# Kernel tuning notes

Measured on AMD Instinct MI355X. Metric: run time of the kernel, lower is better.

The kernel has to match this reference:

```python
import jax, jax.numpy as jnp
import numpy as np

KH = KW = 3
SH = SW = 1
PH = PW = 1


def _im2col(x, kh, kw, sh, sw, ph, pw):
    # x: [N, C, H, W] -> cols: [N, C*kh*kw, H_out*W_out], ordering (C, kh, kw)
    N, C, H, W = x.shape
    H_out = (H + 2 * ph - kh) // sh + 1
    W_out = (W + 2 * pw - kw) // sw + 1
    x_pad = jnp.pad(x, ((0, 0), (0, 0), (ph, ph), (pw, pw)))
    # fixed small loop over kernel offsets (kh*kw = 9), strided slices
    patches = [x_pad[:, :, i:i + sh * H_out:sh, j:j + sw * W_out:sw]
               for i in range(kh) for j in range(kw)]  # each [N, C, H_out, W_out]
    cols = jnp.stack(patches, axis=2)  # [N, C, kh*kw, H_out, W_out]
    cols = cols.reshape(N, C * kh * kw, H_out * W_out)
    return cols, H_out, W_out


def setup_inputs() -> dict:
    key = jax.random.key(0)
    k1, k2, k3 = jax.random.split(key, 3)
    x = jax.random.normal(k1, (16, 128, 56, 56), dtype=jnp.float32)
    weight = jax.random.normal(k2, (256, 128, 3, 3), dtype=jnp.float32) * 0.05
    fan_in = 128 * 3 * 3
    bound = 1.0 / fan_in ** 0.5
    bias = jax.random.uniform(k3, (256,), dtype=jnp.float32, minval=-bound, maxval=bound)
    return {"x": x, "weight": weight, "bias": bias}


def reference(x, weight, bias):
    # im2col unfold + (analog) matmul conv; noise_cfg=None -> plain matmul
    cols, H_out, W_out = _im2col(x, KH, KW, SH, SW, PH, PW)  # [N, K, L]
    N = cols.shape[0]
    Cout = weight.shape[0]
    Wmat = weight.reshape(Cout, -1)  # [Cout, K], K = C*kh*kw
    # y[n, l, o] = sum_k cols[n, k, l] * Wmat[o, k]  (AnalogMatMulFn without noise)
    y = jnp.einsum('nkl,ok->nol', cols, Wmat)  # [N, Cout, L]
    y = y.reshape(N, Cout, H_out, W_out)
    y = y + bias[None, :, None, None]
    return y
```

## Files before the change

### kernel.cpp

```cpp
#include <hip/hip_runtime.h>
#include <hip/hip_bf16.h>
#include <stdint.h>


typedef __attribute__((ext_vector_type(8))) short short8;
typedef __attribute__((ext_vector_type(4))) float floatx4;

__device__ static inline void gload_lds16(const void* g, void* l) {
  typedef const __attribute__((address_space(1))) unsigned int* gp_t;
  typedef __attribute__((address_space(3))) unsigned int* lp_t;
  __builtin_amdgcn_global_load_lds((gp_t)(uintptr_t)g, (lp_t)(uint32_t)(uintptr_t)l,
                                   16, 0, 0);
}

__global__ __launch_bounds__(256)
void pre_kernel(const float* __restrict__ x, const float* __restrict__ wsrc,
                __hip_bfloat16* __restrict__ xp, __hip_bfloat16* __restrict__ wt) {
  const int b = blockIdx.x;
  if (b < 16 * 58) {
    const int n = b / 58, hp = b % 58;
    __hip_bfloat16* dst = xp + (size_t)(n * 58 + hp) * 58 * 128;
    if (hp == 0 || hp == 57) {
      const uint4 z = {0, 0, 0, 0};
      uint4* p = (uint4*)dst;
      for (int i = threadIdx.x; i < 928; i += 256) p[i] = z;
      return;
    }
    const int h = hp - 1;
    __shared__ float tile[128][57];
    const float* src = x + (size_t)n * (128 * 3136) + h * 56;
    for (int i = threadIdx.x; i < 128 * 14; i += 256) {
      const int c = i / 14, q = i - c * 14;
      const float4 v = ((const float4*)(src + (size_t)c * 3136))[q];
      tile[c][4 * q + 0] = v.x;
      tile[c][4 * q + 1] = v.y;
      tile[c][4 * q + 2] = v.z;
      tile[c][4 * q + 3] = v.w;
    }
    __syncthreads();
    if (threadIdx.x < 32) {
      const uint4 z = {0, 0, 0, 0};
      const int col = (threadIdx.x >> 4) * 57;
      ((uint4*)(dst + (size_t)col * 128))[threadIdx.x & 15] = z;
    }
    __hip_bfloat16* di = dst + 128;
    for (int i = threadIdx.x; i < 56 * 16; i += 256) {
      const int w = i >> 4, c8 = (i & 15) * 8;
      union { uint4 u; __hip_bfloat16 hh[8]; } pk;
#pragma unroll
      for (int j = 0; j < 8; ++j) pk.hh[j] = __float2bfloat16(tile[c8 + j][w]);
      *(uint4*)(di + (size_t)w * 128 + c8) = pk.u;
    }
  } else {
    const int base = (b - 928) * 256 + threadIdx.x;
    for (int t = base; t < 256 * 9 * 128; t += 36 * 256) {
      const int e = t & 7;
      const int rr = (t >> 3) & 15;
      const int q = (t >> 7) & 3;
      const int ks = (t >> 9) & 1;
      const int ch = (t >> 10) & 1;
      const int t11 = t >> 11;
      const int kq = t11 % 9;
      const int g = t11 / 9;
      const int cout = g * 16 + rr;
      const int c = ch * 64 + ks * 32 + q * 8 + e;
      wt[t] = __float2bfloat16(wsrc[(size_t)(cout * 128 + c) * 9 + kq]);
    }
  }
}

__global__ __launch_bounds__(256, 3)
void conv_gemm_kernel(const __hip_bfloat16* __restrict__ xp,
                      const __hip_bfloat16* __restrict__ wt,
                      const float* __restrict__ bias,
                      float* __restrict__ out) {
  __shared__ __align__(16) char smem[49152];

  const int tid = threadIdx.x;
  const int lane = tid & 63;
  const int wave = tid >> 6;
  const int col = lane & 15;
  const int quad = lane >> 4;

  const int id = blockIdx.x;
  const int xcd = id & 7;
  const int r = id >> 3;
  const int nt_ = xcd * 98 + r;
  const int n0 = nt_ * 64;

  const int nimg0 = n0 / 3136;
  const int rem0 = n0 - nimg0 * 3136;
  const int hh0 = rem0 / 56;
  const int ww0 = rem0 - hh0 * 56;
  const int P0 = (nimg0 * 58 + hh0) * 58 + ww0;
  const char* pbase = (const char*)xp + (size_t)P0 * 256;

#pragma unroll
  for (int i = 0; i < 12; ++i) {
    const int j = i * 256 + tid;
    const int row = j >> 4;
    const int slot = j & 15;
    gload_lds16(pbase + row * 256 + ((slot ^ (row & 7)) << 4),
                smem + i * 4096 + wave * 1024);
  }

  const char* wtb = (const char*)wt;
  const char* pA = wtb + (size_t)(wave * 4) * 36864 + lane * 16;

  int rbase[4];
#pragma unroll
  for (int nt = 0; nt < 4; ++nt) {
    const int pix = n0 + nt * 16 + col;
    const int ni = pix / 3136;
    const int re = pix - ni * 3136;
    const int ph = re / 56;
    const int pw = re - ph * 56;
    rbase[nt] = (ni * 58 + ph) * 58 + pw - P0;
  }

  floatx4 acc[4][4];
#pragma unroll
  for (int a = 0; a < 4; ++a)
#pragma unroll
    for (int c = 0; c < 4; ++c) acc[a][c] = (floatx4)0.f;

  __syncthreads();

#pragma unroll
  for (int s = 0; s < 18; ++s) {
    const int kq = s >> 1, ch = s & 1;
    const int kh = kq / 3;
    const int tofs = kh * 58 + (kq - kh * 3);
    const int aofs = kq * 4096 + ch * 2048;

    short8 af[4][2];
#pragma unroll
    for (int mt = 0; mt < 4; ++mt)
#pragma unroll
      for (int ks = 0; ks < 2; ++ks)
        af[mt][ks] = *(const short8*)(pA + mt * 36864 + aofs + ks * 1024);

    short8 bf[4][2];
#pragma unroll
    for (int nt = 0; nt < 4; ++nt) {
      const int rowB = rbase[nt] + tofs;
#pragma unroll
      for (int ks = 0; ks < 2; ++ks) {
        const int cB = ch * 8 + ks * 4 + quad;
        const int pos = cB ^ (rowB & 7);
        bf[nt][ks] = *(const short8*)(smem + rowB * 256 + (pos << 4));
      }
    }

#pragma unroll
    for (int ks = 0; ks < 2; ++ks)
#pragma unroll
      for (int mt = 0; mt < 4; ++mt)
#pragma unroll
        for (int nt = 0; nt < 4; ++nt)
          acc[mt][nt] = __builtin_amdgcn_mfma_f32_16x16x32_bf16(
              af[mt][ks], bf[nt][ks], acc[mt][nt], 0, 0, 0);
  }

  const int rb = quad * 4;
#pragma unroll
  for (int nt = 0; nt < 4; ++nt) {
    const int pix = n0 + nt * 16 + col;
    const int nimg = pix / 3136;
    const int rem = pix - nimg * 3136;
    float* op = out + (size_t)nimg * (256 * 3136) + rem;
#pragma unroll
    for (int mt = 0; mt < 4; ++mt) {
      const int mb = wave * 64 + mt * 16 + rb;
#pragma unroll
      for (int rr = 0; rr < 4; ++rr) {
        op[(size_t)(mb + rr) * 3136] = acc[mt][nt][rr] + bias[mb + rr];
      }
    }
  }
}

__global__ __launch_bounds__(256)
void direct_conv_kernel(const float* __restrict__ x, const float* __restrict__ wgt,
                        const float* __restrict__ bias, float* __restrict__ out) {
  const long t = (long)blockIdx.x * 256 + threadIdx.x;
  if (t >= 16L * 256 * 3136) return;
  const int w = t % 56;
  const int h = (t / 56) % 56;
  const int o = (t / 3136) % 256;
  const int n = t / (256L * 3136);
  float s = bias[o];
  for (int c = 0; c < 128; ++c)
    for (int kh = 0; kh < 3; ++kh) {
      const int hh = h + kh - 1;
      if (hh < 0 || hh >= 56) continue;
      for (int kw = 0; kw < 3; ++kw) {
        const int ww = w + kw - 1;
        if (ww < 0 || ww >= 56) continue;
        s += x[((size_t)(n * 128 + c) * 56 + hh) * 56 + ww] *
             wgt[((size_t)(o * 128 + c) * 3 + kh) * 3 + kw];
      }
    }
  out[t] = s;
}

extern "C" void kernel_launch(void* const* d_in, const int* in_sizes, int n_in,
                              void* d_out, int out_size, void* d_ws, size_t ws_size,
                              hipStream_t stream) {
  const float* x = (const float*)d_in[0];
  const float* w = (const float*)d_in[1];
  const float* b = (const float*)d_in[2];
  float* out = (float*)d_out;

  const size_t xp_bytes = (size_t)16 * 58 * 58 * 128 * 2;
  const size_t wt_bytes = (size_t)256 * 9 * 128 * 2;

  if (ws_size >= xp_bytes + wt_bytes) {
    __hip_bfloat16* xp = (__hip_bfloat16*)d_ws;
    __hip_bfloat16* wt = (__hip_bfloat16*)((char*)d_ws + xp_bytes);
    hipLaunchKernelGGL(pre_kernel, dim3(16 * 58 + 36), dim3(256), 0, stream,
                       x, w, xp, wt);
    hipLaunchKernelGGL(conv_gemm_kernel, dim3(784), dim3(256), 0, stream,
                       xp, wt, b, out);
  } else {
    const long total = 16L * 256 * 3136;
    hipLaunchKernelGGL(direct_conv_kernel, dim3((unsigned)((total + 255) / 256)),
                       dim3(256), 0, stream, x, w, b, out);
  }
}
```

Before: 128.8 us.

## Tile output pixels as 8x8 spatial blocks to shrink LDS halo

Each block now covers an 8x8 spatial tile instead of 64 consecutive pixels along rows. The 10x10 halo needs only 100 padded rows in LDS instead of 192, so LDS drops from 48KB to 25KB. Launch bounds are raised to allow 4 blocks per CU. Output stores become strided 8-wide segments rather than 64 contiguous floats, which may reduce write coalescing.

```diff
diff --git a/kernel.cpp b/kernel.cpp
--- a/kernel.cpp
+++ b/kernel.cpp
@@ -69,12 +69,12 @@
   }
 }
 
-__global__ __launch_bounds__(256, 3)
+__global__ __launch_bounds__(256, 4)
 void conv_gemm_kernel(const __hip_bfloat16* __restrict__ xp,
                       const __hip_bfloat16* __restrict__ wt,
                       const float* __restrict__ bias,
                       float* __restrict__ out) {
-  __shared__ __align__(16) char smem[49152];
+  __shared__ __align__(16) char smem[25600];
 
   const int tid = threadIdx.x;
   const int lane = tid & 63;
@@ -85,37 +85,41 @@
   const int id = blockIdx.x;
   const int xcd = id & 7;
   const int r = id >> 3;
-  const int nt_ = xcd * 98 + r;
-  const int n0 = nt_ * 64;
-
-  const int nimg0 = n0 / 3136;
-  const int rem0 = n0 - nimg0 * 3136;
-  const int hh0 = rem0 / 56;
-  const int ww0 = rem0 - hh0 * 56;
-  const int P0 = (nimg0 * 58 + hh0) * 58 + ww0;
-  const char* pbase = (const char*)xp + (size_t)P0 * 256;
-
-#pragma unroll
-  for (int i = 0; i < 12; ++i) {
-    const int j = i * 256 + tid;
-    const int row = j >> 4;
-    const int slot = j & 15;
-    gload_lds16(pbase + row * 256 + ((slot ^ (row & 7)) << 4),
-                smem + i * 4096 + wave * 1024);
+  const int t = xcd * 98 + r;
+  const int nimg = t / 49;
+  const int ti = t - nimg * 49;
+  const int th = ti / 7;
+  const int tw = ti - th * 7;
+  const int h0 = th * 8, w0 = tw * 8;
+
+  const char* pbase = (const char*)xp +
+                      ((size_t)(nimg * 58 + h0) * 58 + w0) * 256;
+
+#pragma unroll
+  for (int i = 0; i < 7; ++i) {
+    if (i < 6 || tid < 64) {
+      const int j = i * 256 + tid;
+      const int row = j >> 4;
+      const int hh = row / 10;
+      const int ww = row - hh * 10;
+      const int slot = j & 15;
+      const int srcb = (slot ^ (row & 7)) << 4;
+      gload_lds16(pbase + (hh * 58 + ww) * 256 + srcb,
+                  smem + i * 4096 + wave * 1024);
+    }
   }
 
   const char* wtb = (const char*)wt;
   const char* pA = wtb + (size_t)(wave * 4) * 36864 + lane * 16;
 
-  int rbase[4];
+  int rbase[4], pixofs[4];
 #pragma unroll
   for (int nt = 0; nt < 4; ++nt) {
-    const int pix = n0 + nt * 16 + col;
-    const int ni = pix / 3136;
-    const int re = pix - ni * 3136;
-    const int ph = re / 56;
-    const int pw = re - ph * 56;
-    rbase[nt] = (ni * 58 + ph) * 58 + pw - P0;
+    const int idx = nt * 16 + col;
+    const int lh = idx >> 3;
+    const int lw = idx & 7;
+    rbase[nt] = lh * 10 + lw;
+    pixofs[nt] = (h0 + lh) * 56 + (w0 + lw);
   }
 
   floatx4 acc[4][4];
@@ -130,7 +134,7 @@
   for (int s = 0; s < 18; ++s) {
     const int kq = s >> 1, ch = s & 1;
     const int kh = kq / 3;
-    const int tofs = kh * 58 + (kq - kh * 3);
+    const int tofs = kh * 10 + (kq - kh * 3);
     const int aofs = kq * 4096 + ch * 2048;
 
     short8 af[4][2];
@@ -162,16 +166,12 @@
               af[mt][ks], bf[nt][ks], acc[mt][nt], 0, 0, 0);
   }
 
-  const int rb = quad * 4;
 #pragma unroll
   for (int nt = 0; nt < 4; ++nt) {
-    const int pix = n0 + nt * 16 + col;
-    const int nimg = pix / 3136;
-    const int rem = pix - nimg * 3136;
-    float* op = out + (size_t)nimg * (256 * 3136) + rem;
+    float* op = out + (size_t)nimg * (256 * 3136) + pixofs[nt];
 #pragma unroll
     for (int mt = 0; mt < 4; ++mt) {
-      const int mb = wave * 64 + mt * 16 + rb;
+      const int mb = wave * 64 + mt * 16 + quad * 4;
 #pragma unroll
       for (int rr = 0; rr < 4; ++rr) {
         op[(size_t)(mb + rr) * 3136] = acc[mt][nt][rr] + bias[mb + rr];
```

After: 183.0 us. +42.1%, slower.
